# Performance work log

Hardware: AMD Instinct MI355X
Metric: run time of the kernel (lower is better)

## Reference

```python
import jax, jax.numpy as jnp
import numpy as np

N = 20000
E = 640000
IN_CH = 256
HID = 128
OUT_CH = 64
HEADS = 8
C1 = HID // HEADS   # 16 per-head dim, layer 1 (concat)
C2 = OUT_CH         # 64 per-head dim, layer 2 (head mean)
NEG_SLOPE = 0.2


def gat_conv(x, edge_index, W, a_src, a_dst, b, concat):
    """PyG GATConv (no self loops, eval mode / no dropout).
    W: [F_in, H*C], a_src/a_dst: [H, C], b: [H*C] or [C]."""
    H, C = a_src.shape
    h = (x @ W).reshape(-1, H, C)                      # [N, H, C]
    s_src = jnp.einsum('nhc,hc->nh', h, a_src)         # [N, H]
    s_dst = jnp.einsum('nhc,hc->nh', h, a_dst)         # [N, H]
    src, dst = edge_index[0], edge_index[1]
    e = jax.nn.leaky_relu(s_src[src] + s_dst[dst], NEG_SLOPE)  # [E, H]
    # segment softmax over incoming edges of each destination node
    m = jax.ops.segment_max(e, dst, num_segments=N)    # [N, H] (-inf for isolated)
    p = jnp.exp(e - m[dst])                            # [E, H]
    z = jax.ops.segment_sum(p, dst, num_segments=N)    # [N, H]
    alpha = p / z[dst]                                 # [E, H]
    out = jax.ops.segment_sum(h[src] * alpha[..., None], dst, num_segments=N)  # [N,H,C]
    out = out.reshape(-1, H * C) if concat else out.mean(axis=1)
    return out + b


def hetero_layer(x, edge_indices, Ws, a_srcs, a_dsts, bs, concat):
    # HeteroConv(aggr='mean') over edge types targeting 'user'
    outs = [gat_conv(x, edge_indices[t], Ws[t], a_srcs[t], a_dsts[t], bs[t], concat)
            for t in range(len(edge_indices))]
    return sum(outs) / len(outs)


def setup_inputs() -> dict:
    key = jax.random.key(0)
    ks = jax.random.split(key, 16)
    g = 0.1
    return {
        'x': jax.random.normal(ks[0], (N, IN_CH), dtype=jnp.float32),
        'edge_index_a': jax.random.randint(ks[1], (2, E), 0, N, dtype=jnp.int32).astype(jnp.int64),
        'edge_index_b': jax.random.randint(ks[2], (2, E), 0, N, dtype=jnp.int32).astype(jnp.int64),
        # layer 1 params, stacked over 2 edge types
        'W1': jax.random.normal(ks[3], (2, IN_CH, HEADS * C1), dtype=jnp.float32) * g,
        'a1_src': jax.random.normal(ks[4], (2, HEADS, C1), dtype=jnp.float32) * g,
        'a1_dst': jax.random.normal(ks[5], (2, HEADS, C1), dtype=jnp.float32) * g,
        'b1': jnp.zeros((2, HEADS * C1), dtype=jnp.float32),
        # layer 2 params
        'W2': jax.random.normal(ks[6], (2, HID, HEADS * C2), dtype=jnp.float32) * g,
        'a2_src': jax.random.normal(ks[7], (2, HEADS, C2), dtype=jnp.float32) * g,
        'a2_dst': jax.random.normal(ks[8], (2, HEADS, C2), dtype=jnp.float32) * g,
        'b2': jnp.zeros((2, C2), dtype=jnp.float32),
        # classifier
        'Wc1': jax.random.normal(ks[9], (OUT_CH, 32), dtype=jnp.float32) * g,
        'bc1': jnp.zeros((32,), dtype=jnp.float32),
        'Wc2': jax.random.normal(ks[10], (32, 2), dtype=jnp.float32) * g,
        'bc2': jnp.zeros((2,), dtype=jnp.float32),
    }


def reference(x, edge_index_a, edge_index_b, W1, a1_src, a1_dst, b1,
              W2, a2_src, a2_dst, b2, Wc1, bc1, Wc2, bc2):
    eis = [edge_index_a, edge_index_b]
    h = hetero_layer(x, eis, W1, a1_src, a1_dst, b1, concat=True)   # [N, 128]
    h = jax.nn.elu(h)  # (dropout is identity in eval mode)
    h = hetero_layer(h, eis, W2, a2_src, a2_dst, b2, concat=False)  # [N, 64]
    h = jax.nn.elu(h)
    logits = jax.nn.relu(h @ Wc1 + bc1) @ Wc2 + bc2                 # [N, 2]
    return logits
```

## Files before the change

### kernel.cpp

```cpp
#include <hip/hip_runtime.h>
#include <hip/hip_bf16.h>
#include <math.h>

#define NN 20000
#define EE 640000
#define NB 157
#define BCAP 5120
#define NBLK 160
#define CHNK 4000

__device__ __forceinline__ void wave_fence() {
  __builtin_amdgcn_wave_barrier();
  asm volatile("s_waitcnt lgkmcnt(0)" ::: "memory");
  __builtin_amdgcn_wave_barrier();
}

__device__ __forceinline__ unsigned pack_bf2(float a, float b) {
  __hip_bfloat162 h2 = __float22bfloat162_rn(make_float2(a, b));
  return *(unsigned*)&h2;
}
__device__ __forceinline__ float2 unpack_bf2(unsigned v) {
  float2 r;
  unsigned lo = v << 16, hi = v & 0xffff0000u;
  r.x = __uint_as_float(lo);
  r.y = __uint_as_float(hi);
  return r;
}

__global__ __launch_bounds__(256) void bin_k(const int* __restrict__ ea,
                                             const int* __restrict__ eb,
                                             int* __restrict__ gcnt,
                                             int* __restrict__ bbuf) {
  int t = blockIdx.y;
  const int* ei = t ? eb : ea;
  int tid = threadIdx.x;
  __shared__ int lh[NB], lbase[NB];
  if (tid < NB) lh[tid] = 0;
  __syncthreads();
  int e0 = blockIdx.x * CHNK;
  int e1 = min(e0 + CHNK, EE);
  int myb[16], myr[16], myv[16];
#pragma unroll
  for (int i = 0; i < 16; ++i) {
    int e = e0 + tid + i * 256;
    if (e < e1) {
      int s = ei[e], d = ei[EE + e];
      int b = d >> 7;
      myb[i] = b;
      myv[i] = (s << 7) | (d & 127);
      myr[i] = atomicAdd(&lh[b], 1);
    } else {
      myb[i] = -1;
    }
  }
  __syncthreads();
  if (tid < NB) {
    int c = lh[tid];
    lbase[tid] = c ? atomicAdd(&gcnt[t * NB + tid], c) : 0;
  }
  __syncthreads();
#pragma unroll
  for (int i = 0; i < 16; ++i) {
    int b = myb[i];
    if (b >= 0) {
      int pos = lbase[b] + myr[i];
      if (pos < BCAP) bbuf[((size_t)t * NB + b) * BCAP + pos] = myv[i];
    }
  }
}

__global__ __launch_bounds__(512) void bscan_k(const int* __restrict__ gcnt,
                                               int* __restrict__ bstart) {
  __shared__ int buf[512];
  int tid = threadIdx.x;
  int t = tid >> 8, b = tid & 255;
  int val = (b < NB) ? gcnt[t * NB + b] : 0;
  buf[tid] = val;
  __syncthreads();
  for (int s = 1; s < 256; s <<= 1) {
    int x = ((tid & 255) >= s) ? buf[tid - s] : 0;
    __syncthreads();
    buf[tid] += x;
    __syncthreads();
  }
  if (b < NB) bstart[t * NB + b] = buf[tid] - val;
}

__global__ __launch_bounds__(256) void build_k(const int* __restrict__ gcnt,
                                               const int* __restrict__ bstart,
                                               const int* __restrict__ bbuf,
                                               int* __restrict__ rowptr,
                                               int* __restrict__ csr) {
  int b = blockIdx.x, t = blockIdx.y;
  int cnt = gcnt[t * NB + b];
  int start = bstart[t * NB + b];
  int n0 = b << 7;
  int nlocal = min(128, NN - n0);
  int tid = threadIdx.x;
  __shared__ int arr[128], lcur[128];
  if (tid < 128) arr[tid] = 0;
  __syncthreads();
  const int* ebuf = bbuf + ((size_t)t * NB + b) * BCAP;
  for (int i = tid; i < cnt; i += 256) atomicAdd(&arr[ebuf[i] & 127], 1);
  __syncthreads();
  int deg = (tid < 128) ? arr[tid] : 0;
  for (int s = 1; s < 128; s <<= 1) {
    int x = (tid < 128 && tid >= s) ? arr[tid - s] : 0;
    __syncthreads();
    if (tid < 128) arr[tid] += x;
    __syncthreads();
  }
  if (tid < nlocal) {
    int incl = arr[tid];
    rowptr[t * (NN + 1) + n0 + tid + 1] = start + incl;
    lcur[tid] = start + incl - deg;
  }
  if (b == 0 && tid == 0) rowptr[t * (NN + 1)] = 0;
  __syncthreads();
  for (int i = tid; i < cnt; i += 256) {
    int v = ebuf[i];
    int pos = atomicAdd(&lcur[v & 127], 1);
    csr[(size_t)t * EE + pos] = v >> 7;
  }
}

template <int NT, int BM, int BN, int BK, int TM, int TN>
__global__ __launch_bounds__(NT) void sgemm_k(const float* __restrict__ A,
                                              const float* __restrict__ B,
                                              float* __restrict__ C, int M, int N, int K,
                                              long long Abs, long long Bbs, long long Cbs,
                                              unsigned* __restrict__ Cb, long long Cbb) {
  A += blockIdx.z * Abs; B += blockIdx.z * Bbs; C += blockIdx.z * Cbs;
  if (Cb) Cb += blockIdx.z * Cbb;
  const int bm = blockIdx.x * BM, bn = blockIdx.y * BN;
  __shared__ float As[BK][BM + 4];
  __shared__ float Bs[BK][BN + 4];
  int tid = threadIdx.x;
  constexpr int TX = BN / TN;
  int tx = tid % TX, ty = tid / TX;
  float acc[TM][TN] = {};
  for (int k0 = 0; k0 < K; k0 += BK) {
#pragma unroll
    for (int i = 0; i < (BM * BK) / (NT * 4); ++i) {
      int idx = tid + i * NT;
      int row = idx / (BK / 4), kq = idx % (BK / 4);
      float4 v = make_float4(0.f, 0.f, 0.f, 0.f);
      int gr = bm + row;
      if (gr < M) v = *(const float4*)&A[(size_t)gr * K + k0 + kq * 4];
      As[kq * 4 + 0][row] = v.x; As[kq * 4 + 1][row] = v.y;
      As[kq * 4 + 2][row] = v.z; As[kq * 4 + 3][row] = v.w;
    }
#pragma unroll
    for (int i = 0; i < (BK * BN) / (NT * 4); ++i) {
      int idx = tid + i * NT;
      int row = idx / (BN / 4), cq = idx % (BN / 4);
      *(float4*)&Bs[row][cq * 4] = *(const float4*)&B[(size_t)(k0 + row) * N + bn + cq * 4];
    }
    __syncthreads();
#pragma unroll
    for (int k = 0; k < BK; ++k) {
      float a[TM], b[TN];
#pragma unroll
      for (int i = 0; i < TM; i += 4) *(float4*)&a[i] = *(float4*)&As[k][ty * TM + i];
#pragma unroll
      for (int j = 0; j < TN; j += 4) *(float4*)&b[j] = *(float4*)&Bs[k][tx * TN + j];
#pragma unroll
      for (int i = 0; i < TM; ++i)
#pragma unroll
        for (int j = 0; j < TN; ++j) acc[i][j] += a[i] * b[j];
    }
    __syncthreads();
  }
#pragma unroll
  for (int i = 0; i < TM; ++i) {
    int gr = bm + ty * TM + i;
    if (gr < M) {
#pragma unroll
      for (int j = 0; j < TN; j += 4)
        *(float4*)&C[(size_t)gr * N + bn + tx * TN + j] = *(float4*)&acc[i][j];
      if (Cb) {
#pragma unroll
        for (int j = 0; j < TN; j += 2)
          Cb[(size_t)gr * (N >> 1) + ((bn + tx * TN + j) >> 1)] = pack_bf2(acc[i][j], acc[i][j + 1]);
      }
    }
  }
}

template <int NT, int BM, int BK, int TM, int TN, int KC>
__global__ __launch_bounds__(NT) void sgemm_splitk_k(const unsigned* __restrict__ Ap,
                                                     const float* __restrict__ B,
                                                     float* __restrict__ P, int M, int K) {
  const int N = 64;
  int t = blockIdx.z;
  Ap += (size_t)t * M * (K >> 1);
  B += (size_t)t * 65536;
  P += ((size_t)t * 4 + blockIdx.y) * M * N;
  const int bm = blockIdx.x * BM;
  const int k0base = blockIdx.y * KC;
  __shared__ float As[BK][BM + 4];
  __shared__ float Bs[BK][N + 4];
  int tid = threadIdx.x;
  constexpr int TX = N / TN;
  int tx = tid % TX, ty = tid / TX;
  float acc[TM][TN] = {};
  for (int k0 = k0base; k0 < k0base + KC; k0 += BK) {
    {
      int row = tid >> 2, q = tid & 3;
      int gr = bm + row;
      uint4 u = make_uint4(0u, 0u, 0u, 0u);
      if (gr < M) u = *(const uint4*)&Ap[(size_t)gr * (K >> 1) + (k0 >> 1) + q * 4];
      float2 f0 = unpack_bf2(u.x), f1 = unpack_bf2(u.y);
      float2 f2 = unpack_bf2(u.z), f3 = unpack_bf2(u.w);
      int kl = q * 8;
      As[kl + 0][row] = f0.x; As[kl + 1][row] = f0.y;
      As[kl + 2][row] = f1.x; As[kl + 3][row] = f1.y;
      As[kl + 4][row] = f2.x; As[kl + 5][row] = f2.y;
      As[kl + 6][row] = f3.x; As[kl + 7][row] = f3.y;
    }
#pragma unroll
    for (int i = 0; i < (BK * N) / (NT * 4); ++i) {
      int idx = tid + i * NT;
      int row = idx / (N / 4), cq = idx % (N / 4);
      *(float4*)&Bs[row][cq * 4] = *(const float4*)&B[(size_t)(k0 + row) * N + cq * 4];
    }
    __syncthreads();
#pragma unroll
    for (int k = 0; k < BK; ++k) {
      float a[TM], b[TN];
#pragma unroll
      for (int i = 0; i < TM; i += 4) *(float4*)&a[i] = *(float4*)&As[k][ty * TM + i];
#pragma unroll
      for (int j = 0; j < TN; j += 4) *(float4*)&b[j] = *(float4*)&Bs[k][tx * TN + j];
#pragma unroll
      for (int i = 0; i < TM; ++i)
#pragma unroll
        for (int j = 0; j < TN; ++j) acc[i][j] += a[i] * b[j];
    }
    __syncthreads();
  }
#pragma unroll
  for (int i = 0; i < TM; ++i) {
    int gr = bm + ty * TM + i;
    if (gr < M) {
#pragma unroll
      for (int j = 0; j < TN; j += 4)
        *(float4*)&P[(size_t)gr * N + tx * TN + j] = *(float4*)&acc[i][j];
    }
  }
}

template <int C>
__global__ void score_k(const float* __restrict__ hf, const float* __restrict__ as_,
                        const float* __restrict__ ad_, float* __restrict__ ss,
                        float* __restrict__ sd) {
  int idx = blockIdx.x * 256 + threadIdx.x;
  if (idx >= 2 * NN * 8) return;
  int t = idx / (NN * 8), r = idx % (NN * 8), n = r / 8, hh = r % 8;
  const int HC = 8 * C;
  const float* hrow = hf + (size_t)t * NN * HC + (size_t)n * HC + hh * C;
  const float* a1 = as_ + t * HC + hh * C;
  const float* a2 = ad_ + t * HC + hh * C;
  float s1 = 0.f, s2 = 0.f;
#pragma unroll
  for (int c = 0; c < C; c += 4) {
    float4 f = *(const float4*)&hrow[c];
    float4 u = *(const float4*)&a1[c];
    float4 w = *(const float4*)&a2[c];
    s1 += f.x * u.x + f.y * u.y + f.z * u.z + f.w * u.w;
    s2 += f.x * w.x + f.y * w.y + f.z * w.z + f.w * w.w;
  }
  ss[idx] = s1; sd[idx] = s2;
}

__device__ __forceinline__ float lrelu(float v) { return v > 0.f ? v : 0.2f * v; }

__global__ __launch_bounds__(256) void aggw1_k(const int* __restrict__ rowptr,
                                               const int* __restrict__ csr,
                                               const float* __restrict__ ssrc,
                                               const float* __restrict__ sdst,
                                               const unsigned* __restrict__ hb,
                                               float* __restrict__ out) {
  int t = blockIdx.y;
  rowptr += t * (NN + 1); csr += (size_t)t * EE;
  ssrc += (size_t)t * NN * 8; sdst += (size_t)t * NN * 8;
  hb += (size_t)t * NN * 64; out += (size_t)t * NN * 128;
  int tid = threadIdx.x, w = tid >> 6, lane = tid & 63;
  int n = blockIdx.x * 4 + w;
  int row = rowptr[n], end = rowptr[n + 1];
  __shared__ int sidx[4][64];
  __shared__ float sexp[4][64][8];
  float4 sda = *(const float4*)&sdst[(size_t)n * 8];
  float4 sdb = *(const float4*)&sdst[(size_t)n * 8 + 4];
  float za_x = 0.f, za_y = 0.f, za_z = 0.f, za_w = 0.f;
  float zb_x = 0.f, zb_y = 0.f, zb_z = 0.f, zb_w = 0.f;
  int hme = lane >> 3;
  float2 acc = make_float2(0.f, 0.f);
  for (int base = row; base < end; base += 64) {
    int cnt = min(64, end - base);
    if (lane < cnt) {
      int s = csr[base + lane];
      sidx[w][lane] = s;
      float4 pa = *(const float4*)&ssrc[(size_t)s * 8];
      float4 pb = *(const float4*)&ssrc[(size_t)s * 8 + 4];
      float4 ea, eb;
      ea.x = __expf(lrelu(pa.x + sda.x)); ea.y = __expf(lrelu(pa.y + sda.y));
      ea.z = __expf(lrelu(pa.z + sda.z)); ea.w = __expf(lrelu(pa.w + sda.w));
      eb.x = __expf(lrelu(pb.x + sdb.x)); eb.y = __expf(lrelu(pb.y + sdb.y));
      eb.z = __expf(lrelu(pb.z + sdb.z)); eb.w = __expf(lrelu(pb.w + sdb.w));
      za_x += ea.x; za_y += ea.y; za_z += ea.z; za_w += ea.w;
      zb_x += eb.x; zb_y += eb.y; zb_z += eb.z; zb_w += eb.w;
      *(float4*)&sexp[w][lane][0] = ea;
      *(float4*)&sexp[w][lane][4] = eb;
    }
    wave_fence();
    for (int e = 0; e < cnt; ++e) {
      int s = sidx[w][e];
      float a = sexp[w][e][hme];
      float2 v = unpack_bf2(hb[(size_t)s * 64 + lane]);
      acc.x += a * v.x; acc.y += a * v.y;
    }
    wave_fence();
  }
#pragma unroll
  for (int off = 32; off; off >>= 1) {
    za_x += __shfl_xor(za_x, off); za_y += __shfl_xor(za_y, off);
    za_z += __shfl_xor(za_z, off); za_w += __shfl_xor(za_w, off);
    zb_x += __shfl_xor(zb_x, off); zb_y += __shfl_xor(zb_y, off);
    zb_z += __shfl_xor(zb_z, off); zb_w += __shfl_xor(zb_w, off);
  }
  float zh[8] = {za_x, za_y, za_z, za_w, zb_x, zb_y, zb_z, zb_w};
  float z = zh[hme];
  float iz = z > 0.f ? 1.f / z : 0.f;
  acc.x *= iz; acc.y *= iz;
  *(float2*)&out[(size_t)n * 128 + lane * 2] = acc;
}

__global__ void combine1_k(const float* __restrict__ oa, const float* __restrict__ ob,
                           const float* __restrict__ b1, float* __restrict__ hmid,
                           unsigned* __restrict__ hmidb) {
  int idx = blockIdx.x * 256 + threadIdx.x;
  if (idx >= NN * 64) return;
  int n = idx >> 6, j2 = idx & 63, j = j2 * 2;
  float2 va = *(const float2*)&oa[(size_t)n * 128 + j];
  float2 vb = *(const float2*)&ob[(size_t)n * 128 + j];
  float vx = 0.5f * ((va.x + b1[j]) + (vb.x + b1[128 + j]));
  float vy = 0.5f * ((va.y + b1[j + 1]) + (vb.y + b1[128 + j + 1]));
  vx = vx > 0.f ? vx : (__expf(vx) - 1.f);
  vy = vy > 0.f ? vy : (__expf(vy) - 1.f);
  *(float2*)&hmid[(size_t)n * 128 + j] = make_float2(vx, vy);
  hmidb[idx] = pack_bf2(vx, vy);
}

__global__ void fold2_k(const float* __restrict__ W2, const float* __restrict__ a2s,
                        const float* __restrict__ a2d, float* __restrict__ wsf,
                        float* __restrict__ wdf) {
  int idx = blockIdx.x * 256 + threadIdx.x;
  if (idx >= 2048) return;
  int t = idx >> 10, r = idx & 1023, hh = r >> 7, k = r & 127;
  const float* wrow = W2 + (size_t)t * 65536 + (size_t)k * 512 + hh * 64;
  const float* as = a2s + t * 512 + hh * 64;
  const float* ad = a2d + t * 512 + hh * 64;
  float s1 = 0.f, s2 = 0.f;
  for (int c = 0; c < 64; ++c) { s1 += wrow[c] * as[c]; s2 += wrow[c] * ad[c]; }
  wsf[idx] = s1; wdf[idx] = s2;
}

__global__ void foldB_k(const float* __restrict__ W2, float* __restrict__ Bmat) {
  int idx = blockIdx.x * 256 + threadIdx.x;
  if (idx >= 131072) return;
  int t = idx >> 16, r = idx & 65535, rowr = r >> 6, c = r & 63;
  int hh = rowr >> 7, k = rowr & 127;
  Bmat[idx] = 0.125f * W2[(size_t)t * 65536 + (size_t)k * 512 + hh * 64 + c];
}

__global__ void score2_k(const float* __restrict__ hmid, const float* __restrict__ wsf,
                         const float* __restrict__ wdf, float* __restrict__ ss,
                         float* __restrict__ sdo) {
  int idx = blockIdx.x * 256 + threadIdx.x;
  if (idx >= NN * 8) return;
  int n = idx >> 3, hh = idx & 7;
  const float* hm = hmid + (size_t)n * 128;
  const float* w0s = wsf + (size_t)hh * 128;
  const float* w0d = wdf + (size_t)hh * 128;
  const float* w1s = wsf + (size_t)(8 + hh) * 128;
  const float* w1d = wdf + (size_t)(8 + hh) * 128;
  float s0s = 0.f, s0d = 0.f, s1s = 0.f, s1d = 0.f;
#pragma unroll
  for (int c = 0; c < 128; c += 4) {
    float4 f = *(const float4*)&hm[c];
    float4 a = *(const float4*)&w0s[c];
    float4 b = *(const float4*)&w0d[c];
    float4 u = *(const float4*)&w1s[c];
    float4 v = *(const float4*)&w1d[c];
    s0s += f.x * a.x + f.y * a.y + f.z * a.z + f.w * a.w;
    s0d += f.x * b.x + f.y * b.y + f.z * b.z + f.w * b.w;
    s1s += f.x * u.x + f.y * u.y + f.z * u.z + f.w * u.w;
    s1d += f.x * v.x + f.y * v.y + f.z * v.z + f.w * v.w;
  }
  ss[idx] = s0s; sdo[idx] = s0d;
  ss[NN * 8 + idx] = s1s; sdo[NN * 8 + idx] = s1d;
}

__global__ __launch_bounds__(256) void aggw2_k(const int* __restrict__ rowptr,
                                               const int* __restrict__ csr,
                                               const float* __restrict__ ssrc,
                                               const float* __restrict__ sdst,
                                               const unsigned* __restrict__ hmidb,
                                               unsigned* __restrict__ aggp) {
  int t = blockIdx.y;
  rowptr += t * (NN + 1); csr += (size_t)t * EE;
  ssrc += (size_t)t * NN * 8; sdst += (size_t)t * NN * 8;
  aggp += (size_t)t * NN * 512;
  int tid = threadIdx.x, w = tid >> 6, lane = tid & 63;
  int n = blockIdx.x * 4 + w;
  int row = rowptr[n], end = rowptr[n + 1];
  __shared__ int sidx[4][64];
  __shared__ float sexp[4][64][8];
  float4 sda = *(const float4*)&sdst[(size_t)n * 8];
  float4 sdb = *(const float4*)&sdst[(size_t)n * 8 + 4];
  float za_x = 0.f, za_y = 0.f, za_z = 0.f, za_w = 0.f;
  float zb_x = 0.f, zb_y = 0.f, zb_z = 0.f, zb_w = 0.f;
  float2 acc[8];
#pragma unroll
  for (int i = 0; i < 8; ++i) acc[i] = make_float2(0.f, 0.f);
  for (int base = row; base < end; base += 64) {
    int cnt = min(64, end - base);
    if (lane < cnt) {
      int s = csr[base + lane];
      sidx[w][lane] = s;
      float4 pa = *(const float4*)&ssrc[(size_t)s * 8];
      float4 pb = *(const float4*)&ssrc[(size_t)s * 8 + 4];
      float4 ea, eb;
      ea.x = __expf(lrelu(pa.x + sda.x)); ea.y = __expf(lrelu(pa.y + sda.y));
      ea.z = __expf(lrelu(pa.z + sda.z)); ea.w = __expf(lrelu(pa.w + sda.w));
      eb.x = __expf(lrelu(pb.x + sdb.x)); eb.y = __expf(lrelu(pb.y + sdb.y));
      eb.z = __expf(lrelu(pb.z + sdb.z)); eb.w = __expf(lrelu(pb.w + sdb.w));
      za_x += ea.x; za_y += ea.y; za_z += ea.z; za_w += ea.w;
      zb_x += eb.x; zb_y += eb.y; zb_z += eb.z; zb_w += eb.w;
      *(float4*)&sexp[w][lane][0] = ea;
      *(float4*)&sexp[w][lane][4] = eb;
    }
    wave_fence();
    for (int e = 0; e < cnt; ++e) {
      int s = sidx[w][e];
      float4 ea = *(const float4*)&sexp[w][e][0];
      float4 eb = *(const float4*)&sexp[w][e][4];
      float2 v = unpack_bf2(hmidb[(size_t)s * 64 + lane]);
      acc[0].x += ea.x * v.x; acc[0].y += ea.x * v.y;
      acc[1].x += ea.y * v.x; acc[1].y += ea.y * v.y;
      acc[2].x += ea.z * v.x; acc[2].y += ea.z * v.y;
      acc[3].x += ea.w * v.x; acc[3].y += ea.w * v.y;
      acc[4].x += eb.x * v.x; acc[4].y += eb.x * v.y;
      acc[5].x += eb.y * v.x; acc[5].y += eb.y * v.y;
      acc[6].x += eb.z * v.x; acc[6].y += eb.z * v.y;
      acc[7].x += eb.w * v.x; acc[7].y += eb.w * v.y;
    }
    wave_fence();
  }
#pragma unroll
  for (int off = 32; off; off >>= 1) {
    za_x += __shfl_xor(za_x, off); za_y += __shfl_xor(za_y, off);
    za_z += __shfl_xor(za_z, off); za_w += __shfl_xor(za_w, off);
    zb_x += __shfl_xor(zb_x, off); zb_y += __shfl_xor(zb_y, off);
    zb_z += __shfl_xor(zb_z, off); zb_w += __shfl_xor(zb_w, off);
  }
  float zh[8] = {za_x, za_y, za_z, za_w, zb_x, zb_y, zb_z, zb_w};
#pragma unroll
  for (int i = 0; i < 8; ++i) {
    float z = zh[i];
    float iz = z > 0.f ? 1.f / z : 0.f;
    aggp[(size_t)n * 512 + i * 64 + lane] = pack_bf2(acc[i].x * iz, acc[i].y * iz);
  }
}

__global__ void combine2p_k(const float* __restrict__ P, const float* __restrict__ b2,
                            float* __restrict__ feat) {
  int idx = blockIdx.x * 256 + threadIdx.x;
  if (idx >= NN * 16) return;
  int n = idx >> 4, j = (idx & 15) * 4;
  const size_t SZ = (size_t)NN * 64;
  size_t o = (size_t)n * 64 + j;
  float4 sa = make_float4(0.f, 0.f, 0.f, 0.f), sb = sa;
#pragma unroll
  for (int k = 0; k < 4; ++k) {
    float4 va = *(const float4*)&P[k * SZ + o];
    float4 vb = *(const float4*)&P[(4 + k) * SZ + o];
    sa.x += va.x; sa.y += va.y; sa.z += va.z; sa.w += va.w;
    sb.x += vb.x; sb.y += vb.y; sb.z += vb.z; sb.w += vb.w;
  }
  float4 ba = *(const float4*)&b2[j];
  float4 bb = *(const float4*)&b2[64 + j];
  float4 v;
  v.x = 0.5f * ((sa.x + ba.x) + (sb.x + bb.x));
  v.y = 0.5f * ((sa.y + ba.y) + (sb.y + bb.y));
  v.z = 0.5f * ((sa.z + ba.z) + (sb.z + bb.z));
  v.w = 0.5f * ((sa.w + ba.w) + (sb.w + bb.w));
  v.x = v.x > 0.f ? v.x : (__expf(v.x) - 1.f);
  v.y = v.y > 0.f ? v.y : (__expf(v.y) - 1.f);
  v.z = v.z > 0.f ? v.z : (__expf(v.z) - 1.f);
  v.w = v.w > 0.f ? v.w : (__expf(v.w) - 1.f);
  *(float4*)&feat[o] = v;
}

__global__ __launch_bounds__(256) void cls_k(const float* __restrict__ feat,
                                             const float* __restrict__ Wc1,
                                             const float* __restrict__ bc1,
                                             const float* __restrict__ Wc2,
                                             const float* __restrict__ bc2,
                                             float* __restrict__ out) {
  __shared__ float w1[64 * 32];
  __shared__ float w2[64];
  __shared__ float b1s[32], b2s[2];
  __shared__ float fs[8 * 64];
  __shared__ float hs[8 * 32];
  int tid = threadIdx.x;
  for (int i = tid; i < 2048; i += 256) w1[i] = Wc1[i];
  if (tid < 64) w2[tid] = Wc2[tid];
  if (tid < 32) b1s[tid] = bc1[tid];
  if (tid < 2) b2s[tid] = bc2[tid];
  int nbase = blockIdx.x * 8;
  for (int i = tid; i < 512; i += 256) fs[i] = feat[(size_t)nbase * 64 + i];
  __syncthreads();
  int local = tid >> 5, tt = tid & 31;
  const float* f = fs + local * 64;
  float acc = b1s[tt];
#pragma unroll
  for (int c = 0; c < 64; ++c) acc += f[c] * w1[c * 32 + tt];
  hs[local * 32 + tt] = fmaxf(acc, 0.f);
  __syncthreads();
  if (tid < 16) {
    int l = tid >> 1, j = tid & 1;
    float o = b2s[j];
#pragma unroll
    for (int i = 0; i < 32; ++i) o += hs[l * 32 + i] * w2[i * 2 + j];
    out[(size_t)(nbase + l) * 2 + j] = o;
  }
}

extern "C" void kernel_launch(void* const* d_in, const int* in_sizes, int n_in,
                              void* d_out, int out_size, void* d_ws, size_t ws_size,
                              hipStream_t stream) {
  const float* x   = (const float*)d_in[0];
  const int* eia   = (const int*)d_in[1];
  const int* eib   = (const int*)d_in[2];
  const float* W1  = (const float*)d_in[3];
  const float* a1s = (const float*)d_in[4];
  const float* a1d = (const float*)d_in[5];
  const float* b1  = (const float*)d_in[6];
  const float* W2  = (const float*)d_in[7];
  const float* a2s = (const float*)d_in[8];
  const float* a2d = (const float*)d_in[9];
  const float* b2  = (const float*)d_in[10];
  const float* Wc1 = (const float*)d_in[11];
  const float* bc1 = (const float*)d_in[12];
  const float* Wc2 = (const float*)d_in[13];
  const float* bc2 = (const float*)d_in[14];
  float* out = (float*)d_out;

  char* ws = (char*)d_ws;
  size_t off = 0;
  auto alloc = [&](size_t bytes) -> char* {
    char* p = ws + off;
    off += (bytes + 255) & ~(size_t)255;
    return p;
  };
  int* gcnt       = (int*)alloc((size_t)2 * NB * 4);
  int* bstart     = (int*)alloc((size_t)2 * NB * 4);
  int* bbuf       = (int*)alloc((size_t)2 * NB * BCAP * 4);
  int* rowptr     = (int*)alloc((size_t)2 * (NN + 1) * 4);
  int* csr        = (int*)alloc((size_t)2 * EE * 4);
  float* h1       = (float*)alloc((size_t)2 * NN * 128 * 4);
  unsigned* h1b   = (unsigned*)alloc((size_t)2 * NN * 64 * 4);
  float* s1s      = (float*)alloc((size_t)2 * NN * 8 * 4);
  float* s1d      = (float*)alloc((size_t)2 * NN * 8 * 4);
  float* o1       = (float*)alloc((size_t)2 * NN * 128 * 4);
  float* hmid     = (float*)alloc((size_t)NN * 128 * 4);
  unsigned* hmidb = (unsigned*)alloc((size_t)NN * 64 * 4);
  float* wsf      = (float*)alloc((size_t)2048 * 4);
  float* wdf      = (float*)alloc((size_t)2048 * 4);
  float* Bmat     = (float*)alloc((size_t)131072 * 4);
  float* s2s      = (float*)alloc((size_t)2 * NN * 8 * 4);
  float* s2d      = (float*)alloc((size_t)2 * NN * 8 * 4);
  unsigned* aggp  = (unsigned*)alloc((size_t)2 * NN * 512 * 4);
  float* pbuf     = (float*)alloc((size_t)8 * NN * 64 * 4);
  float* feat     = (float*)alloc((size_t)NN * 64 * 4);

  hipMemsetAsync(gcnt, 0, (size_t)2 * NB * 4, stream);
  bin_k<<<dim3(NBLK, 2), 256, 0, stream>>>(eia, eib, gcnt, bbuf);
  bscan_k<<<1, 512, 0, stream>>>(gcnt, bstart);
  build_k<<<dim3(NB, 2), 256, 0, stream>>>(gcnt, bstart, bbuf, rowptr, csr);

  fold2_k<<<8, 256, 0, stream>>>(W2, a2s, a2d, wsf, wdf);
  foldB_k<<<512, 256, 0, stream>>>(W2, Bmat);

  sgemm_k<256, 64, 64, 32, 4, 4><<<dim3((NN + 63) / 64, 2, 2), 256, 0, stream>>>(
      x, W1, h1, NN, 128, 256, 0LL, 256LL * 128, (long long)NN * 128, h1b, (long long)NN * 64);
  score_k<16><<<(2 * NN * 8 + 255) / 256, 256, 0, stream>>>(h1, a1s, a1d, s1s, s1d);
  aggw1_k<<<dim3(NN / 4, 2), 256, 0, stream>>>(rowptr, csr, s1s, s1d, h1b, o1);
  combine1_k<<<(NN * 64 + 255) / 256, 256, 0, stream>>>(o1, o1 + (size_t)NN * 128, b1, hmid, hmidb);

  score2_k<<<(NN * 8 + 255) / 256, 256, 0, stream>>>(hmid, wsf, wdf, s2s, s2d);
  aggw2_k<<<dim3(NN / 4, 2), 256, 0, stream>>>(rowptr, csr, s2s, s2d, hmidb, aggp);
  sgemm_splitk_k<256, 64, 32, 4, 4, 256><<<dim3((NN + 63) / 64, 4, 2), 256, 0, stream>>>(
      aggp, Bmat, pbuf, NN, 1024);
  combine2p_k<<<(NN * 16 + 255) / 256, 256, 0, stream>>>(pbuf, b2, feat);

  cls_k<<<NN / 8, 256, 0, stream>>>(feat, Wc1, bc1, Wc2, bc2, out);
}
```

Measured before the change: 453.3 us.

## Fuse small kernels into neighbours and add nontemporal loads/stores in aggregation

Folds the bucket scan into build_k (each block redoes the 157-entry scan), merges the two W2 folding kernels into one launch, and fuses the split-K partial reduction, bias and ELU into the classifier kernel. That removes three launches and the feat intermediate buffer. It also marks CSR index loads and the aggregation output stores nontemporal and uses an ext_vector accumulator. The trade-off is redundant scan work per block and scalar (non-vectorised) partial-sum reads in cls_k.

```diff
diff --git a/kernel.cpp b/kernel.cpp
--- a/kernel.cpp
+++ b/kernel.cpp
@@ -8,6 +8,8 @@
 #define BCAP 5120
 #define NBLK 160
 #define CHNK 4000
+
+typedef float v2f __attribute__((ext_vector_type(2)));
 
 __device__ __forceinline__ void wave_fence() {
   __builtin_amdgcn_wave_barrier();
@@ -69,34 +71,29 @@
   }
 }
 
-__global__ __launch_bounds__(512) void bscan_k(const int* __restrict__ gcnt,
-                                               int* __restrict__ bstart) {
-  __shared__ int buf[512];
-  int tid = threadIdx.x;
-  int t = tid >> 8, b = tid & 255;
-  int val = (b < NB) ? gcnt[t * NB + b] : 0;
-  buf[tid] = val;
-  __syncthreads();
-  for (int s = 1; s < 256; s <<= 1) {
-    int x = ((tid & 255) >= s) ? buf[tid - s] : 0;
-    __syncthreads();
-    buf[tid] += x;
-    __syncthreads();
-  }
-  if (b < NB) bstart[t * NB + b] = buf[tid] - val;
-}
-
 __global__ __launch_bounds__(256) void build_k(const int* __restrict__ gcnt,
-                                               const int* __restrict__ bstart,
                                                const int* __restrict__ bbuf,
                                                int* __restrict__ rowptr,
                                                int* __restrict__ csr) {
   int b = blockIdx.x, t = blockIdx.y;
+  int tid = threadIdx.x;
+  __shared__ int sb[256];
+  __shared__ int sstart;
+  int bv = (tid < NB) ? gcnt[t * NB + tid] : 0;
+  sb[tid] = bv;
+  __syncthreads();
+  for (int s = 1; s < 256; s <<= 1) {
+    int x = (tid >= s) ? sb[tid - s] : 0;
+    __syncthreads();
+    sb[tid] += x;
+    __syncthreads();
+  }
+  if (tid == b) sstart = sb[tid] - bv;
+  __syncthreads();
+  int start = sstart;
   int cnt = gcnt[t * NB + b];
-  int start = bstart[t * NB + b];
   int n0 = b << 7;
   int nlocal = min(128, NN - n0);
-  int tid = threadIdx.x;
   __shared__ int arr[128], lcur[128];
   if (tid < 128) arr[tid] = 0;
   __syncthreads();
@@ -295,11 +292,11 @@
   float za_x = 0.f, za_y = 0.f, za_z = 0.f, za_w = 0.f;
   float zb_x = 0.f, zb_y = 0.f, zb_z = 0.f, zb_w = 0.f;
   int hme = lane >> 3;
-  float2 acc = make_float2(0.f, 0.f);
+  v2f acc = {0.f, 0.f};
   for (int base = row; base < end; base += 64) {
     int cnt = min(64, end - base);
     if (lane < cnt) {
-      int s = csr[base + lane];
+      int s = __builtin_nontemporal_load(&csr[base + lane]);
       sidx[w][lane] = s;
       float4 pa = *(const float4*)&ssrc[(size_t)s * 8];
       float4 pb = *(const float4*)&ssrc[(size_t)s * 8 + 4];
@@ -317,8 +314,9 @@
     for (int e = 0; e < cnt; ++e) {
       int s = sidx[w][e];
       float a = sexp[w][e][hme];
-      float2 v = unpack_bf2(hb[(size_t)s * 64 + lane]);
-      acc.x += a * v.x; acc.y += a * v.y;
+      float2 vf = unpack_bf2(hb[(size_t)s * 64 + lane]);
+      v2f v = {vf.x, vf.y};
+      acc += a * v;
     }
     wave_fence();
   }
@@ -332,8 +330,8 @@
   float zh[8] = {za_x, za_y, za_z, za_w, zb_x, zb_y, zb_z, zb_w};
   float z = zh[hme];
   float iz = z > 0.f ? 1.f / z : 0.f;
-  acc.x *= iz; acc.y *= iz;
-  *(float2*)&out[(size_t)n * 128 + lane * 2] = acc;
+  __builtin_nontemporal_store(acc.x * iz, &out[(size_t)n * 128 + lane * 2]);
+  __builtin_nontemporal_store(acc.y * iz, &out[(size_t)n * 128 + lane * 2 + 1]);
 }
 
 __global__ void combine1_k(const float* __restrict__ oa, const float* __restrict__ ob,
@@ -352,26 +350,24 @@
   hmidb[idx] = pack_bf2(vx, vy);
 }
 
-__global__ void fold2_k(const float* __restrict__ W2, const float* __restrict__ a2s,
-                        const float* __restrict__ a2d, float* __restrict__ wsf,
-                        float* __restrict__ wdf) {
+__global__ void fold_k(const float* __restrict__ W2, const float* __restrict__ a2s,
+                       const float* __restrict__ a2d, float* __restrict__ wsf,
+                       float* __restrict__ wdf, float* __restrict__ Bmat) {
   int idx = blockIdx.x * 256 + threadIdx.x;
-  if (idx >= 2048) return;
-  int t = idx >> 10, r = idx & 1023, hh = r >> 7, k = r & 127;
-  const float* wrow = W2 + (size_t)t * 65536 + (size_t)k * 512 + hh * 64;
-  const float* as = a2s + t * 512 + hh * 64;
-  const float* ad = a2d + t * 512 + hh * 64;
-  float s1 = 0.f, s2 = 0.f;
-  for (int c = 0; c < 64; ++c) { s1 += wrow[c] * as[c]; s2 += wrow[c] * ad[c]; }
-  wsf[idx] = s1; wdf[idx] = s2;
-}
-
-__global__ void foldB_k(const float* __restrict__ W2, float* __restrict__ Bmat) {
-  int idx = blockIdx.x * 256 + threadIdx.x;
-  if (idx >= 131072) return;
-  int t = idx >> 16, r = idx & 65535, rowr = r >> 6, c = r & 63;
-  int hh = rowr >> 7, k = rowr & 127;
-  Bmat[idx] = 0.125f * W2[(size_t)t * 65536 + (size_t)k * 512 + hh * 64 + c];
+  if (idx < 131072) {
+    int t = idx >> 16, r = idx & 65535, rowr = r >> 6, c = r & 63;
+    int hh = rowr >> 7, k = rowr & 127;
+    Bmat[idx] = 0.125f * W2[(size_t)t * 65536 + (size_t)k * 512 + hh * 64 + c];
+  }
+  if (idx < 2048) {
+    int t = idx >> 10, r = idx & 1023, hh = r >> 7, k = r & 127;
+    const float* wrow = W2 + (size_t)t * 65536 + (size_t)k * 512 + hh * 64;
+    const float* as = a2s + t * 512 + hh * 64;
+    const float* ad = a2d + t * 512 + hh * 64;
+    float s1 = 0.f, s2 = 0.f;
+    for (int c = 0; c < 64; ++c) { s1 += wrow[c] * as[c]; s2 += wrow[c] * ad[c]; }
+    wsf[idx] = s1; wdf[idx] = s2;
+  }
 }
 
 __global__ void score2_k(const float* __restrict__ hmid, const float* __restrict__ wsf,
@@ -427,7 +423,7 @@
   for (int base = row; base < end; base += 64) {
     int cnt = min(64, end - base);
     if (lane < cnt) {
-      int s = csr[base + lane];
+      int s = __builtin_nontemporal_load(&csr[base + lane]);
       sidx[w][lane] = s;
       float4 pa = *(const float4*)&ssrc[(size_t)s * 8];
       float4 pb = *(const float4*)&ssrc[(size_t)s * 8 + 4];
@@ -470,40 +466,13 @@
   for (int i = 0; i < 8; ++i) {
     float z = zh[i];
     float iz = z > 0.f ? 1.f / z : 0.f;
-    aggp[(size_t)n * 512 + i * 64 + lane] = pack_bf2(acc[i].x * iz, acc[i].y * iz);
-  }
-}
-
-__global__ void combine2p_k(const float* __restrict__ P, const float* __restrict__ b2,
-                            float* __restrict__ feat) {
-  int idx = blockIdx.x * 256 + threadIdx.x;
-  if (idx >= NN * 16) return;
-  int n = idx >> 4, j = (idx & 15) * 4;
-  const size_t SZ = (size_t)NN * 64;
-  size_t o = (size_t)n * 64 + j;
-  float4 sa = make_float4(0.f, 0.f, 0.f, 0.f), sb = sa;
-#pragma unroll
-  for (int k = 0; k < 4; ++k) {
-    float4 va = *(const float4*)&P[k * SZ + o];
-    float4 vb = *(const float4*)&P[(4 + k) * SZ + o];
-    sa.x += va.x; sa.y += va.y; sa.z += va.z; sa.w += va.w;
-    sb.x += vb.x; sb.y += vb.y; sb.z += vb.z; sb.w += vb.w;
-  }
-  float4 ba = *(const float4*)&b2[j];
-  float4 bb = *(const float4*)&b2[64 + j];
-  float4 v;
-  v.x = 0.5f * ((sa.x + ba.x) + (sb.x + bb.x));
-  v.y = 0.5f * ((sa.y + ba.y) + (sb.y + bb.y));
-  v.z = 0.5f * ((sa.z + ba.z) + (sb.z + bb.z));
-  v.w = 0.5f * ((sa.w + ba.w) + (sb.w + bb.w));
-  v.x = v.x > 0.f ? v.x : (__expf(v.x) - 1.f);
-  v.y = v.y > 0.f ? v.y : (__expf(v.y) - 1.f);
-  v.z = v.z > 0.f ? v.z : (__expf(v.z) - 1.f);
-  v.w = v.w > 0.f ? v.w : (__expf(v.w) - 1.f);
-  *(float4*)&feat[o] = v;
-}
-
-__global__ __launch_bounds__(256) void cls_k(const float* __restrict__ feat,
+    __builtin_nontemporal_store(pack_bf2(acc[i].x * iz, acc[i].y * iz),
+                                &aggp[(size_t)n * 512 + i * 64 + lane]);
+  }
+}
+
+__global__ __launch_bounds__(256) void cls_k(const float* __restrict__ P,
+                                             const float* __restrict__ b2,
                                              const float* __restrict__ Wc1,
                                              const float* __restrict__ bc1,
                                              const float* __restrict__ Wc2,
@@ -520,7 +489,19 @@
   if (tid < 32) b1s[tid] = bc1[tid];
   if (tid < 2) b2s[tid] = bc2[tid];
   int nbase = blockIdx.x * 8;
-  for (int i = tid; i < 512; i += 256) fs[i] = feat[(size_t)nbase * 64 + i];
+  const size_t SZ = (size_t)NN * 64;
+  for (int i = tid; i < 512; i += 256) {
+    size_t o = (size_t)nbase * 64 + i;
+    float sa = 0.f, sb = 0.f;
+#pragma unroll
+    for (int k = 0; k < 4; ++k) {
+      sa += P[k * SZ + o];
+      sb += P[(4 + k) * SZ + o];
+    }
+    int c = i & 63;
+    float v = 0.5f * ((sa + b2[c]) + (sb + b2[64 + c]));
+    fs[i] = v > 0.f ? v : (__expf(v) - 1.f);
+  }
   __syncthreads();
   int local = tid >> 5, tt = tid & 31;
   const float* f = fs + local * 64;
@@ -566,7 +547,6 @@
     return p;
   };
   int* gcnt       = (int*)alloc((size_t)2 * NB * 4);
-  int* bstart     = (int*)alloc((size_t)2 * NB * 4);
   int* bbuf       = (int*)alloc((size_t)2 * NB * BCAP * 4);
   int* rowptr     = (int*)alloc((size_t)2 * (NN + 1) * 4);
   int* csr        = (int*)alloc((size_t)2 * EE * 4);
@@ -584,15 +564,12 @@
   float* s2d      = (float*)alloc((size_t)2 * NN * 8 * 4);
   unsigned* aggp  = (unsigned*)alloc((size_t)2 * NN * 512 * 4);
   float* pbuf     = (float*)alloc((size_t)8 * NN * 64 * 4);
-  float* feat     = (float*)alloc((size_t)NN * 64 * 4);
 
   hipMemsetAsync(gcnt, 0, (size_t)2 * NB * 4, stream);
   bin_k<<<dim3(NBLK, 2), 256, 0, stream>>>(eia, eib, gcnt, bbuf);
-  bscan_k<<<1, 512, 0, stream>>>(gcnt, bstart);
-  build_k<<<dim3(NB, 2), 256, 0, stream>>>(gcnt, bstart, bbuf, rowptr, csr);
-
-  fold2_k<<<8, 256, 0, stream>>>(W2, a2s, a2d, wsf, wdf);
-  foldB_k<<<512, 256, 0, stream>>>(W2, Bmat);
+  build_k<<<dim3(NB, 2), 256, 0, stream>>>(gcnt, bbuf, rowptr, csr);
+
+  fold_k<<<512, 256, 0, stream>>>(W2, a2s, a2d, wsf, wdf, Bmat);
 
   sgemm_k<256, 64, 64, 32, 4, 4><<<dim3((NN + 63) / 64, 2, 2), 256, 0, stream>>>(
       x, W1, h1, NN, 128, 256, 0LL, 256LL * 128, (long long)NN * 128, h1b, (long long)NN * 64);
@@ -604,7 +581,6 @@
   aggw2_k<<<dim3(NN / 4, 2), 256, 0, stream>>>(rowptr, csr, s2s, s2d, hmidb, aggp);
   sgemm_splitk_k<256, 64, 32, 4, 4, 256><<<dim3((NN + 63) / 64, 4, 2), 256, 0, stream>>>(
       aggp, Bmat, pbuf, NN, 1024);
-  combine2p_k<<<(NN * 16 + 255) / 256, 256, 0, stream>>>(pbuf, b2, feat);
-
-  cls_k<<<NN / 8, 256, 0, stream>>>(feat, Wc1, bc1, Wc2, bc2, out);
-}
+
+  cls_k<<<NN / 8, 256, 0, stream>>>(pbuf, b2, Wc1, bc1, Wc2, bc2, out);
+}
```

After: 464.9 us. +2.6%, slower.
